# Optimization experiments

Measured on AMD Instinct MI355X. Metric: run time of the kernel, lower is better.

## Reference

```python
import jax, jax.numpy as jnp
import numpy as np

N_CELLS_PER_SIDE = 16
MAX_K = 32
N_HEADS = 8
CHUNK = 128

_NEIGHBOR_OFFSETS = jnp.array([[-1, -1], [-1, 0], [-1, 1], [0, -1], [0, 0], [0, 1], [1, -1], [1, 0], [1, 1]], dtype=jnp.int32)


def cell_lookup(query_pos, cell_map, pos_min, pos_range):
    B, S, _ = query_pos.shape
    mpc = cell_map.shape[1]
    normalized = (query_pos - pos_min) / pos_range
    cell_xy = jnp.clip((normalized * N_CELLS_PER_SIDE).astype(jnp.int32), 0, N_CELLS_PER_SIDE - 1)
    nb = jnp.clip(cell_xy[:, :, None, :] + _NEIGHBOR_OFFSETS[None, None, :, :], 0, N_CELLS_PER_SIDE - 1)
    nidx = nb[..., 0] * N_CELLS_PER_SIDE + nb[..., 1]
    cand = cell_map[nidx].reshape(B, S, 9 * mpc)
    valid = cand >= 0
    return jnp.where(valid, cand, 0), valid


def threshold_gate(scores, tau, max_k):
    raw = scores - tau
    gate = jnp.where(raw > 0, raw, 1e-8 * jnp.exp(raw))
    eg = jnp.exp(gate) - 1.0
    k = min(max_k, scores.shape[-1])
    tv, _ = jax.lax.top_k(eg, k)
    eg = jnp.where(eg >= tv[:, :, -1:], eg, 0.0)
    gs = eg.sum(axis=-1, keepdims=True) + 1e-8
    strength = jnp.tanh(eg.max(axis=-1, keepdims=True))
    return eg / gs * strength


def setup_inputs() -> dict:
    key = jax.random.key(0)
    ks = jax.random.split(key, 16)
    B, S, D, N, P = 2, 1024, 512, 4096, 2
    n_cells, mpc = N_CELLS_PER_SIDE ** 2, 32
    return {
        "x": jax.random.normal(ks[0], (B, S, D), jnp.float32),
        "qk_pos": jax.random.uniform(ks[1], (B, S, P), jnp.float32),
        "v_pos": jax.random.uniform(ks[2], (B, S, P), jnp.float32),
        "tau_Q": jax.random.uniform(ks[3], (B, S, 1), jnp.float32),
        "tau_K": jax.random.uniform(ks[4], (B, S, 1), jnp.float32),
        "tau_V": jax.random.uniform(ks[5], (B, S, 1), jnp.float32),
        "qk_neurons": jax.random.normal(ks[6], (N, D), jnp.float32) / np.float32(np.sqrt(D)),
        "v_neurons": jax.random.normal(ks[7], (N, D), jnp.float32) / np.float32(np.sqrt(D)),
        "npos_qk": jax.random.uniform(ks[8], (N, P), jnp.float32),
        "npos_v": jax.random.uniform(ks[9], (N, P), jnp.float32),
        "cell_map_qk": jax.random.randint(ks[10], (n_cells, mpc), 0, N, jnp.int32),
        "cell_map_v": jax.random.randint(ks[11], (n_cells, mpc), 0, N, jnp.int32),
        "pos_min": jnp.zeros((P,), jnp.float32),
        "pos_range": jnp.ones((P,), jnp.float32),
        "expand_O": jax.random.normal(ks[12], (D, D), jnp.float32) * 0.02,
    }


def reference(x, qk_pos, v_pos, tau_Q, tau_K, tau_V, qk_neurons, v_neurons, npos_qk, npos_v, cell_map_qk, cell_map_v, pos_min, pos_range, expand_O):
    B, S, D = x.shape
    # full-sequence spatial cell lookup (small int tensors)
    ci_qk, m_qk = cell_lookup(qk_pos, cell_map_qk, pos_min, pos_range)
    ci_v, m_v = cell_lookup(v_pos, cell_map_v, pos_min, pos_range)
    ci_qk = jax.lax.stop_gradient(ci_qk)
    ci_v = jax.lax.stop_gradient(ci_v)
    nc = S // CHUNK  # S chosen divisible by CHUNK (no padding path needed)

    def chunks(a):
        return a.reshape(B, nc, CHUNK, *a.shape[2:]).swapaxes(0, 1)

    inp = tuple(map(chunks, (x, qk_pos, v_pos, tau_Q, tau_K, tau_V, ci_qk, m_qk, ci_v, m_v)))

    def step(carry, c):
        x_c, qkp, vp, tq, tk, tv, i_qk, mk, i_v, mv = c
        cand_qk = qk_neurons[i_qk]  # [B,C,n_cand,D]
        cand_v = v_neurons[i_v]
        act_qk = jnp.einsum('bsd,bsnd->bsn', x_c, cand_qk)
        act_v = jnp.einsum('bsd,bsnd->bsn', x_c, cand_v)
        s_qk = jnp.where(mk, act_qk, -1e9)
        s_v = jnp.where(mv, act_v, -1e9)
        gQ = threshold_gate(s_qk, tq, MAX_K)
        gK = threshold_gate(s_qk, tk, MAX_K)
        gV = threshold_gate(s_v, tv, MAX_K)
        Q_c = jnp.einsum('bsn,bsnd->bsd', act_qk * gQ * mk, cand_qk)
        K_c = jnp.einsum('bsn,bsnd->bsd', act_qk * gK * mk, cand_qk)
        V_c = jnp.einsum('bsn,bsnd->bsd', act_v * gV * mv, cand_v)
        pd_qk = jnp.sum((qkp[:, :, None, :] - npos_qk[i_qk]) ** 2, axis=-1)
        pl_qk = (jax.lax.stop_gradient(gQ) * pd_qk * mk).sum() / (mk.sum() + 1e-8)
        pd_v = jnp.sum((vp[:, :, None, :] - npos_v[i_v]) ** 2, axis=-1)
        pl_v = (jax.lax.stop_gradient(gV) * pd_v * mv).sum() / (mv.sum() + 1e-8)
        return carry, (Q_c, K_c, V_c, pl_qk + pl_v)

    _, (Qs, Ks, Vs, pls) = jax.lax.scan(step, 0, inp)

    def merge(a):
        return a.swapaxes(0, 1).reshape(B, S, D)

    Q, K, V = merge(Qs), merge(Ks), merge(Vs)
    pos_loss = pls.mean()  # == sum / n_chunks

    dh = D // N_HEADS
    Qh = Q.reshape(B, S, N_HEADS, dh).transpose(0, 2, 1, 3)
    Kh = K.reshape(B, S, N_HEADS, dh).transpose(0, 2, 1, 3)
    Vh = V.reshape(B, S, N_HEADS, dh).transpose(0, 2, 1, 3)
    scores = jnp.einsum('bhsd,bhtd->bhst', Qh, Kh) / jnp.sqrt(jnp.float32(dh))
    causal = jnp.tril(jnp.ones((S, S), dtype=jnp.bool_))
    scores = jnp.where(causal, scores, jnp.finfo(scores.dtype).min)
    attn = jax.nn.softmax(scores, axis=-1)
    out = jnp.einsum('bhst,bhtd->bhsd', attn, Vh)
    out = out.transpose(0, 2, 1, 3).reshape(B, S, D)
    out = out @ expand_O
    return out, pos_loss
```

## Files before the change

### kernel.cpp

```cpp
#include <hip/hip_runtime.h>
#include <math.h>

#define B_ 2
#define S_ 1024
#define D_ 512
#define N_ 4096
#define H_ 8
#define DH_ 64
#define NCAND 288
#define TOPK 32
#define NTOK (B_*S_)
#define NG2 1152

#define NROWS 16384
#define NSLOT_BH 8704
#define NSLOTS (16*NSLOT_BH)

typedef __attribute__((ext_vector_type(8))) short short8;
typedef __attribute__((ext_vector_type(4))) float f32x4;

__device__ __forceinline__ float wave_sum(float v) {
    #pragma unroll
    for (int o = 32; o; o >>= 1) v += __shfl_xor(v, o);
    return v;
}
__device__ __forceinline__ float wave_max(float v) {
    #pragma unroll
    for (int o = 32; o; o >>= 1) v = fmaxf(v, __shfl_xor(v, o));
    return v;
}
__device__ __forceinline__ ushort f2b_rn(float f) {
    unsigned u = __float_as_uint(f);
    return (ushort)((u + 0x7FFFu + ((u >> 16) & 1u)) >> 16);
}
__device__ __forceinline__ float b2f(ushort h) {
    return __uint_as_float(((unsigned)h) << 16);
}
__device__ __forceinline__ int swzi(int row, int c8) {
    return row * 64 + ((c8 ^ (row & 7)) << 3);
}

__global__ __launch_bounds__(1024) void sort_tokens_kernel(
    const float* __restrict__ qk_pos, const float* __restrict__ v_pos,
    const float* __restrict__ pos_min, const float* __restrict__ pos_range,
    int* __restrict__ order_qk, int* __restrict__ order_v,
    int2* __restrict__ desc_qk, int2* __restrict__ desc_v,
    float* __restrict__ posacc)
{
    __shared__ int hist[256], tmp[256], offs[256], startc[256], gcnt[256];
    const int t = threadIdx.x;
    const int pass = blockIdx.x;
    if (pass == 0 && t < 32) posacc[t] = 0.f;
    const float pm0 = pos_min[0], pm1 = pos_min[1];
    const float pr0 = pos_range[0], pr1 = pos_range[1];
    const float* pos = pass ? v_pos : qk_pos;
    int* order = pass ? order_v : order_qk;
    int2* desc = pass ? desc_v : desc_qk;
    if (t < NG2) desc[t] = make_int2(0, 0);
    if (t + 1024 < NG2) desc[t + 1024] = make_int2(0, 0);
    if (t < 256) hist[t] = 0;
    __syncthreads();
    int cell[2];
    #pragma unroll
    for (int k = 0; k < 2; k++) {
        int tok = t + k * 1024;
        float p0 = pos[tok * 2], p1 = pos[tok * 2 + 1];
        int cx = min(max((int)((p0 - pm0) / pr0 * 16.f), 0), 15);
        int cy = min(max((int)((p1 - pm1) / pr1 * 16.f), 0), 15);
        cell[k] = cx * 16 + cy;
        atomicAdd(&hist[cell[k]], 1);
    }
    __syncthreads();
    if (t < 256) tmp[t] = hist[t];
    __syncthreads();
    for (int d = 1; d < 256; d <<= 1) {
        int v = 0;
        if (t < 256 && t >= d) v = tmp[t - d];
        __syncthreads();
        if (t < 256) tmp[t] += v;
        __syncthreads();
    }
    if (t < 256) {
        startc[t] = tmp[t] - hist[t];
        offs[t]   = startc[t];
        gcnt[t]   = (hist[t] + 1) >> 1;
    }
    __syncthreads();
    #pragma unroll
    for (int k = 0; k < 2; k++) {
        int tok = t + k * 1024;
        int p = atomicAdd(&offs[cell[k]], 1);
        order[p] = tok;
    }
    __syncthreads();
    if (t < 256) tmp[t] = gcnt[t];
    __syncthreads();
    for (int d = 1; d < 256; d <<= 1) {
        int v = 0;
        if (t < 256 && t >= d) v = tmp[t - d];
        __syncthreads();
        if (t < 256) tmp[t] += v;
        __syncthreads();
    }
    if (t < 256) {
        int g0 = tmp[t] - gcnt[t];
        for (int k = 0; k < gcnt[t]; k++)
            desc[g0 + k] = make_int2(startc[t] + 2 * k, min(2, hist[t] - 2 * k));
    }
}

__global__ __launch_bounds__(256) void qkv_fused(
    const int2* __restrict__ desc_qk, const int* __restrict__ order_qk,
    const int2* __restrict__ desc_v,  const int* __restrict__ order_v,
    const float* __restrict__ x,
    const float* __restrict__ qk_pos, const float* __restrict__ v_pos,
    const float* __restrict__ tauQ, const float* __restrict__ tauK,
    const float* __restrict__ tauV,
    const float* __restrict__ qk_neurons, const float* __restrict__ v_neurons,
    const float* __restrict__ npos_qk, const float* __restrict__ npos_v,
    const int* __restrict__ cm_qk, const int* __restrict__ cm_v,
    const float* __restrict__ pos_min, const float* __restrict__ pos_range,
    float* __restrict__ Q, float* __restrict__ K, float* __restrict__ V,
    float* __restrict__ posacc)
{
    const int bid = blockIdx.x;
    const int role = bid & 1;
    const int g = bid >> 1;
    const int gid = (g & 7) * 144 + (g >> 3);
    const int2 dsc = role ? desc_v[gid] : desc_qk[gid];
    const int gstart = dsc.x, count = dsc.y;
    if (count == 0) return;

    const int*   order   = role ? order_v   : order_qk;
    const float* pose    = role ? v_pos     : qk_pos;
    const float* neurons = role ? v_neurons : qk_neurons;
    const float* npos    = role ? npos_v    : npos_qk;
    const int*   cmap    = role ? cm_v      : cm_qk;

    __shared__ int   idx[NCAND];
    __shared__ float msk[NCAND];
    __shared__ float act[2][NCAND];
    __shared__ int   ci[2][NCAND];
    __shared__ float cw1[2][NCAND], cw2[2][NCAND];
    __shared__ int   toks[2], cnt2[2];
    __shared__ float red[2][2][4];
    __shared__ float redc;

    const int t = threadIdx.x, wid = t >> 6, lane = t & 63;
    const int sub = lane & 15, grp = lane >> 4;
    if (t < 2) { toks[t] = order[gstart + min(t, count - 1)]; cnt2[t] = 0; }
    __syncthreads();
    const int token0 = toks[0];

    const float pm0 = pos_min[0], pm1 = pos_min[1];
    const float pr0 = pos_range[0], pr1 = pos_range[1];
    {
        const float p0 = pose[token0 * 2], p1 = pose[token0 * 2 + 1];
        const int cx = min(max((int)((p0 - pm0) / pr0 * 16.f), 0), 15);
        const int cy = min(max((int)((p1 - pm1) / pr1 * 16.f), 0), 15);
        for (int c = t; c < NCAND; c += 256) {
            int o = c >> 5, ms = c & 31;
            int nx = min(max(cx + o / 3 - 1, 0), 15), ny = min(max(cy + o % 3 - 1, 0), 15);
            int cand = cmap[(nx * 16 + ny) * 32 + ms];
            idx[c] = cand >= 0 ? cand : 0;
            msk[c] = cand >= 0 ? 1.f : 0.f;
        }
    }
    __syncthreads();

    float4 xr0[8], xr1[8];
    {
        const float4* xp0 = (const float4*)(x + (size_t)toks[0] * D_);
        const float4* xp1 = (const float4*)(x + (size_t)toks[1] * D_);
        #pragma unroll
        for (int k = 0; k < 8; k++) {
            xr0[k] = xp0[k * 16 + sub];
            xr1[k] = xp1[k * 16 + sub];
        }
    }

    const int cb = wid * 72;
    for (int u = 0; u < 72; u += 4) {
        const int c = cb + u + grp;
        const float4* rp = (const float4*)(neurons + (size_t)idx[c] * D_);
        float a0 = 0.f, a1 = 0.f, b0 = 0.f, b1 = 0.f;
        #pragma unroll
        for (int k = 0; k < 8; k += 2) {
            float4 r0 = rp[k * 16 + sub];
            float4 r1 = rp[(k + 1) * 16 + sub];
            a0 += xr0[k].x*r0.x + xr0[k].y*r0.y + xr0[k].z*r0.z + xr0[k].w*r0.w;
            a1 += xr1[k].x*r0.x + xr1[k].y*r0.y + xr1[k].z*r0.z + xr1[k].w*r0.w;
            b0 += xr0[k+1].x*r1.x + xr0[k+1].y*r1.y + xr0[k+1].z*r1.z + xr0[k+1].w*r1.w;
            b1 += xr1[k+1].x*r1.x + xr1[k+1].y*r1.y + xr1[k+1].z*r1.z + xr1[k+1].w*r1.w;
        }
        float f0 = a0 + b0, f1 = a1 + b1;
        #pragma unroll
        for (int o = 1; o <= 8; o <<= 1) {
            f0 += __shfl_xor(f0, o);
            f1 += __shfl_xor(f1, o);
        }
        if (sub == 0) {
            const float mv = msk[c];
            act[0][c] = (mv != 0.f) ? f0 : -1e9f;
            act[1][c] = (mv != 0.f) ? f1 : -1e9f;
        }
    }
    __syncthreads();

    const int tk = wid >> 1, sw = wid & 1, tt = t & 127;
    const int token = toks[tk];

    if (sw == 0) {
        unsigned ej[5];
        #pragma unroll
        for (int k = 0; k < 5; k++) {
            int j = lane + 64 * k;
            float f = (j < NCAND) ? act[tk][j] : -1e30f;
            unsigned uu = __float_as_uint(f);
            ej[k] = (uu & 0x80000000u) ? ~uu : (uu | 0x80000000u);
        }
        unsigned T = 0u;
        for (int bit = 31; bit >= 0; bit--) {
            const unsigned cand = T | (1u << bit);
            int c = 0;
            #pragma unroll
            for (int k = 0; k < 5; k++)
                c += __popcll(__ballot(ej[k] >= cand));
            if (c >= TOPK) T = cand;
        }
        int base = 0;
        const unsigned long long below = (lane == 0) ? 0ull
                                       : (~0ull >> (64 - lane));
        #pragma unroll
        for (int k = 0; k < 5; k++) {
            const unsigned long long mk2 = __ballot(ej[k] >= T);
            if (ej[k] >= T) {
                int pos = base + __popcll(mk2 & below);
                ci[tk][pos] = lane + 64 * k;
            }
            base += __popcll(mk2);
        }
        if (lane == 0) cnt2[tk] = base;
    }
    if (wid == 0) {
        float cmv = 0.f;
        for (int c = lane; c < NCAND; c += 64) cmv += msk[c];
        cmv = wave_sum(cmv);
        if (lane == 0) redc = cmv;
    }
    __syncthreads();
    const float cm = redc;
    const int n = cnt2[tk];

    if (role == 0) {
        const float tq = tauQ[token], tkk = tauK[token];
        float sQ = 0.f, sK = 0.f, mQ = 0.f, mK = 0.f;
        for (int p = tt; p < n; p += 128) {
            float s = act[tk][ci[tk][p]];
            float rq = s - tq;
            float gq = (rq > 0.f) ? rq : 1e-8f * __expf(rq);
            float egq = __expf(gq) - 1.f;
            float rk = s - tkk;
            float gk = (rk > 0.f) ? rk : 1e-8f * __expf(rk);
            float egk = __expf(gk) - 1.f;
            cw1[tk][p] = egq; cw2[tk][p] = egk;
            sQ += egq; sK += egk;
            mQ = fmaxf(mQ, egq); mK = fmaxf(mK, egk);
        }
        sQ = wave_sum(sQ); mQ = wave_max(mQ);
        sK = wave_sum(sK); mK = wave_max(mK);
        if (lane == 0) {
            red[tk][sw][0] = sQ; red[tk][sw][1] = mQ;
            red[tk][sw][2] = sK; red[tk][sw][3] = mK;
        }
        __syncthreads();
        const float scQ = tanhf(fmaxf(red[tk][0][1], red[tk][1][1]))
                        / (red[tk][0][0] + red[tk][1][0] + 1e-8f);
        const float scK = tanhf(fmaxf(red[tk][0][3], red[tk][1][3]))
                        / (red[tk][0][2] + red[tk][1][2] + 1e-8f);
        __syncthreads();

        const float qp0 = pose[token * 2], qp1 = pose[token * 2 + 1];
        float plq = 0.f;
        for (int p = tt; p < n; p += 128) {
            int e = ci[tk][p];
            int id = idx[e];
            float m = msk[e], a = act[tk][e];
            float gq = cw1[tk][p] * scQ;
            cw1[tk][p] = a * gq * m;
            cw2[tk][p] = a * cw2[tk][p] * scK * m;
            ci[tk][p] = id;
            float d0 = qp0 - npos[id * 2], d1 = qp1 - npos[id * 2 + 1];
            plq += gq * (d0 * d0 + d1 * d1) * m;
        }
        plq = wave_sum(plq);
        if (lane == 0) red[tk][sw][0] = plq;
        __syncthreads();
        if (tt == 0 && tk < count) {
            int chunk = (token & 1023) >> 7;
            atomicAdd(&posacc[chunk], red[tk][0][0] + red[tk][1][0]);
            atomicAdd(&posacc[8 + chunk], cm);
        }

        if (tk < count) {
            float4 qa = {0,0,0,0}, ka = {0,0,0,0};
            int p = 0;
            for (; p + 1 < n; p += 2) {
                const float4 rA = *(const float4*)(neurons + (size_t)ci[tk][p] * D_ + tt * 4);
                const float4 rB = *(const float4*)(neurons + (size_t)ci[tk][p + 1] * D_ + tt * 4);
                const float wA = cw1[tk][p], bA = cw2[tk][p];
                const float wB = cw1[tk][p + 1], bB = cw2[tk][p + 1];
                qa.x += wA * rA.x + wB * rB.x; qa.y += wA * rA.y + wB * rB.y;
                qa.z += wA * rA.z + wB * rB.z; qa.w += wA * rA.w + wB * rB.w;
                ka.x += bA * rA.x + bB * rB.x; ka.y += bA * rA.y + bB * rB.y;
                ka.z += bA * rA.z + bB * rB.z; ka.w += bA * rA.w + bB * rB.w;
            }
            if (p < n) {
                const float4 rA = *(const float4*)(neurons + (size_t)ci[tk][p] * D_ + tt * 4);
                const float wA = cw1[tk][p], bA = cw2[tk][p];
                qa.x += wA * rA.x; qa.y += wA * rA.y; qa.z += wA * rA.z; qa.w += wA * rA.w;
                ka.x += bA * rA.x; ka.y += bA * rA.y; ka.z += bA * rA.z; ka.w += bA * rA.w;
            }
            *(float4*)(Q + (size_t)token * D_ + tt * 4) = qa;
            *(float4*)(K + (size_t)token * D_ + tt * 4) = ka;
        }
    } else {
        const float tv = tauV[token];
        float sV = 0.f, mV = 0.f;
        for (int p = tt; p < n; p += 128) {
            float s = act[tk][ci[tk][p]];
            float rv = s - tv;
            float gv = (rv > 0.f) ? rv : 1e-8f * __expf(rv);
            float egv = __expf(gv) - 1.f;
            cw1[tk][p] = egv;
            sV += egv; mV = fmaxf(mV, egv);
        }
        sV = wave_sum(sV); mV = wave_max(mV);
        if (lane == 0) { red[tk][sw][0] = sV; red[tk][sw][1] = mV; }
        __syncthreads();
        const float scV = tanhf(fmaxf(red[tk][0][1], red[tk][1][1]))
                        / (red[tk][0][0] + red[tk][1][0] + 1e-8f);
        __syncthreads();

        const float vp0 = pose[token * 2], vp1 = pose[token * 2 + 1];
        float plv = 0.f;
        for (int p = tt; p < n; p += 128) {
            int e = ci[tk][p];
            int id = idx[e];
            float m = msk[e], a = act[tk][e];
            float gv = cw1[tk][p] * scV;
            cw1[tk][p] = a * gv * m;
            ci[tk][p] = id;
            float d0 = vp0 - npos[id * 2], d1 = vp1 - npos[id * 2 + 1];
            plv += gv * (d0 * d0 + d1 * d1) * m;
        }
        plv = wave_sum(plv);
        if (lane == 0) red[tk][sw][0] = plv;
        __syncthreads();
        if (tt == 0 && tk < count) {
            int chunk = (token & 1023) >> 7;
            atomicAdd(&posacc[16 + chunk], red[tk][0][0] + red[tk][1][0]);
            atomicAdd(&posacc[24 + chunk], cm);
        }

        if (tk < count) {
            float4 va = {0,0,0,0};
            int p = 0;
            for (; p + 1 < n; p += 2) {
                const float4 rA = *(const float4*)(neurons + (size_t)ci[tk][p] * D_ + tt * 4);
                const float4 rB = *(const float4*)(neurons + (size_t)ci[tk][p + 1] * D_ + tt * 4);
                const float wA = cw1[tk][p], wB = cw1[tk][p + 1];
                va.x += wA * rA.x + wB * rB.x; va.y += wA * rA.y + wB * rB.y;
                va.z += wA * rA.z + wB * rB.z; va.w += wA * rA.w + wB * rB.w;
            }
            if (p < n) {
                const float4 rA = *(const float4*)(neurons + (size_t)ci[tk][p] * D_ + tt * 4);
                const float wA = cw1[tk][p];
                va.x += wA * rA.x; va.y += wA * rA.y; va.z += wA * rA.z; va.w += wA * rA.w;
            }
            *(float4*)(V + (size_t)token * D_ + tt * 4) = va;
        }
    }
}

__global__ __launch_bounds__(256) void wprep_kernel(
    const float* __restrict__ W, ushort* __restrict__ Wth, ushort* __restrict__ Wtl)
{
    __shared__ float tile[64][65];
    const int bx = blockIdx.x & 7, by = blockIdx.x >> 3;
    const int t = threadIdx.x;
    const int r = t >> 4, c4 = (t & 15) * 4;
    #pragma unroll
    for (int rr = 0; rr < 64; rr += 16) {
        const float4 v = *(const float4*)(W + (size_t)(by * 64 + rr + r) * 512 + bx * 64 + c4);
        *(float4*)&tile[rr + r][c4] = v;
    }
    __syncthreads();
    #pragma unroll
    for (int cc = 0; cc < 64; cc += 16) {
        const int c = cc + r;
        ushort h[4], l[4];
        #pragma unroll
        for (int i = 0; i < 4; i++) {
            float f = tile[c4 + i][c];
            h[i] = f2b_rn(f);
            l[i] = f2b_rn(f - b2f(h[i]));
        }
        *(uint2*)&Wth[(size_t)(bx * 64 + c) * 512 + by * 64 + c4] = *(uint2*)h;
        *(uint2*)&Wtl[(size_t)(bx * 64 + c) * 512 + by * 64 + c4] = *(uint2*)l;
    }
}

__global__ __launch_bounds__(256, 2) void attn_partial_kernel(
    const float* __restrict__ Q, const float* __restrict__ K,
    const float* __restrict__ V,
    float* __restrict__ pm, float* __restrict__ pl, float* __restrict__ po)
{
    const int xx = blockIdx.x & 7;
    int kq = blockIdx.x >> 3;
    const int bh = xx + 8 * (kq >= 72);
    kq = (kq >= 72) ? kq - 72 : kq;
    int rblk = 0;
    while (kq >= 2 * (rblk + 1)) { kq -= 2 * (rblk + 1); rblk++; }
    const int sp = kq;
    const int b = bh >> 3, h = bh & 7;
    const int j0 = sp * 64;
    const int rbase = rblk * 128;

    __shared__ __align__(16) ushort sKhi[64 * 64], sKlo[64 * 64];
    __shared__ __align__(16) ushort sVthi[64 * 64], sVtlo[64 * 64];
    __shared__ __align__(16) float sPool[8192];

    const int t = threadIdx.x;
    const int w = t >> 6, lane = t & 63;
    const int g = lane >> 4, ln = lane & 15;

    {
        const int srow = t >> 2, scol = (t & 3) << 4;
        const float* Kg = K + ((size_t)(b * S_ + j0 + srow)) * D_ + h * DH_ + scol;
        const float* Vg = V + ((size_t)(b * S_ + j0 + srow)) * D_ + h * DH_ + scol;
        union { float4 f4[4]; float f[16]; } kf, vf;
        kf.f4[0] = *(const float4*)(Kg);
        kf.f4[1] = *(const float4*)(Kg + 4);
        kf.f4[2] = *(const float4*)(Kg + 8);
        kf.f4[3] = *(const float4*)(Kg + 12);
        vf.f4[0] = *(const float4*)(Vg);
        vf.f4[1] = *(const float4*)(Vg + 4);
        vf.f4[2] = *(const float4*)(Vg + 8);
        vf.f4[3] = *(const float4*)(Vg + 12);
        union { uint4 d[2]; ushort u[16]; } uh, ul;
        #pragma unroll
        for (int i = 0; i < 16; i++) {
            uh.u[i] = f2b_rn(kf.f[i]);
            ul.u[i] = f2b_rn(kf.f[i] - b2f(uh.u[i]));
        }
        const int c8 = (t & 3) << 1;
        *(uint4*)&sKhi[swzi(srow, c8)]     = uh.d[0];
        *(uint4*)&sKhi[swzi(srow, c8 + 1)] = uh.d[1];
        *(uint4*)&sKlo[swzi(srow, c8)]     = ul.d[0];
        *(uint4*)&sKlo[swzi(srow, c8 + 1)] = ul.d[1];
        #pragma unroll
        for (int i = 0; i < 16; i++) sPool[srow * 65 + scol + i] = vf.f[i];
    }
    __syncthreads();
    {
        const int drow = t >> 2, kcol = (t & 3) << 4;
        union { uint4 d[2]; ushort u[16]; } uh, ul;
        #pragma unroll
        for (int i = 0; i < 16; i++) {
            const float f = sPool[(kcol + i) * 65 + drow];
            uh.u[i] = f2b_rn(f);
            ul.u[i] = f2b_rn(f - b2f(uh.u[i]));
        }
        const int c8 = (t & 3) << 1;
        *(uint4*)&sVthi[swzi(drow, c8)]     = uh.d[0];
        *(uint4*)&sVthi[swzi(drow, c8 + 1)] = uh.d[1];
        *(uint4*)&sVtlo[swzi(drow, c8)]     = ul.d[0];
        *(uint4*)&sVtlo[swzi(drow, c8 + 1)] = ul.d[1];
    }
    __syncthreads();

    const int wrow = rbase + w * 32;
    if (wrow + 31 < j0) return;

    ushort* sPw = (ushort*)sPool + w * 4096;

    short8 qhi[2][2], qlo[2][2];
    #pragma unroll
    for (int qt = 0; qt < 2; qt++) {
        const int qrow = wrow + qt * 16 + ln;
        const float* Qg = Q + ((size_t)(b * S_ + qrow)) * D_ + h * DH_ + g * 8;
        #pragma unroll
        for (int ds = 0; ds < 2; ds++) {
            union { float4 f4[2]; float f[8]; } qf;
            qf.f4[0] = *(const float4*)(Qg + ds * 32);
            qf.f4[1] = *(const float4*)(Qg + ds * 32 + 4);
            union { short8 v; ushort u[8]; } uh, ul;
            #pragma unroll
            for (int i = 0; i < 8; i++) {
                uh.u[i] = f2b_rn(qf.f[i]);
                ul.u[i] = f2b_rn(qf.f[i] - b2f(uh.u[i]));
            }
            qhi[qt][ds] = uh.v; qlo[qt][ds] = ul.v;
        }
    }

    const f32x4 fzero = {0.f, 0.f, 0.f, 0.f};
    f32x4 sT[2][4];
    #pragma unroll
    for (int qt = 0; qt < 2; qt++)
        #pragma unroll
        for (int kt = 0; kt < 4; kt++)
            sT[qt][kt] = fzero;
    #pragma unroll
    for (int ds = 0; ds < 2; ds++) {
        #pragma unroll
        for (int kt = 0; kt < 4; kt++) {
            const int krow = kt * 16 + ln;
            const short8 khi = *(const short8*)&sKhi[swzi(krow, ds * 4 + g)];
            const short8 klo = *(const short8*)&sKlo[swzi(krow, ds * 4 + g)];
            #pragma unroll
            for (int qt = 0; qt < 2; qt++) {
                sT[qt][kt] = __builtin_amdgcn_mfma_f32_16x16x32_bf16(khi, qhi[qt][ds], sT[qt][kt], 0, 0, 0);
                sT[qt][kt] = __builtin_amdgcn_mfma_f32_16x16x32_bf16(khi, qlo[qt][ds], sT[qt][kt], 0, 0, 0);
                sT[qt][kt] = __builtin_amdgcn_mfma_f32_16x16x32_bf16(klo, qhi[qt][ds], sT[qt][kt], 0, 0, 0);
            }
        }
    }

    #pragma unroll
    for (int qt = 0; qt < 2; qt++) {
        const int qg = wrow + qt * 16 + ln;
        float pv[16];
        float mq = -1e30f;
        #pragma unroll
        for (int kt = 0; kt < 4; kt++)
            #pragma unroll
            for (int r = 0; r < 4; r++) {
                const int kg = j0 + kt * 16 + g * 4 + r;
                float s = sT[qt][kt][r] * 0.125f;
                s = (kg <= qg) ? s : -1e30f;
                pv[kt * 4 + r] = s;
                mq = fmaxf(mq, s);
            }
        mq = fmaxf(mq, __shfl_xor(mq, 16));
        mq = fmaxf(mq, __shfl_xor(mq, 32));
        const float base = (mq < -1e29f) ? 0.f : mq;
        float lq = 0.f;
        #pragma unroll
        for (int i = 0; i < 16; i++) {
            const float e = __expf(pv[i] - base);
            pv[i] = e;
            lq += e;
        }
        lq += __shfl_xor(lq, 16);
        lq += __shfl_xor(lq, 32);

        const int qrow = qt * 16 + ln;
        #pragma unroll
        for (int kt = 0; kt < 4; kt++) {
            union { uint2 d; ushort u[4]; } h4, l4;
            #pragma unroll
            for (int r = 0; r < 4; r++) {
                const float f = pv[kt * 4 + r];
                h4.u[r] = f2b_rn(f);
                l4.u[r] = f2b_rn(f - b2f(h4.u[r]));
            }
            const int c8 = kt * 2 + (g >> 1);
            const int idx = qrow * 64 + ((c8 ^ (qrow & 7)) << 3) + ((g & 1) << 2);
            *(uint2*)&sPw[idx] = h4.d;
            *(uint2*)&sPw[2048 + idx] = l4.d;
        }
        if (g == 0 && qg >= j0) {
            const int gr = qg >> 6;
            const size_t slot = (size_t)bh * NSLOT_BH + 32 * gr * (gr + 1)
                              + (size_t)(qg & 63) * (gr + 1) + sp;
            pm[slot] = mq; pl[slot] = lq;
        }
    }

    f32x4 ot[4][2];
    #pragma unroll
    for (int dt = 0; dt < 4; dt++)
        #pragma unroll
        for (int qt = 0; qt < 2; qt++)
            ot[dt][qt] = fzero;
    #pragma unroll
    for (int ks = 0; ks < 2; ks++) {
        short8 pfh[2], pfl[2];
        #pragma unroll
        for (int qt = 0; qt < 2; qt++) {
            const int qrow = qt * 16 + ln;
            const int idx = qrow * 64 + (((ks * 4 + g) ^ (qrow & 7)) << 3);
            pfh[qt] = *(const short8*)&sPw[idx];
            pfl[qt] = *(const short8*)&sPw[2048 + idx];
        }
        #pragma unroll
        for (int dt = 0; dt < 4; dt++) {
            const int drow = dt * 16 + ln;
            const short8 vh = *(const short8*)&sVthi[swzi(drow, ks * 4 + g)];
            const short8 vl = *(const short8*)&sVtlo[swzi(drow, ks * 4 + g)];
            #pragma unroll
            for (int qt = 0; qt < 2; qt++) {
                ot[dt][qt] = __builtin_amdgcn_mfma_f32_16x16x32_bf16(vh, pfh[qt], ot[dt][qt], 0, 0, 0);
                ot[dt][qt] = __builtin_amdgcn_mfma_f32_16x16x32_bf16(vh, pfl[qt], ot[dt][qt], 0, 0, 0);
                ot[dt][qt] = __builtin_amdgcn_mfma_f32_16x16x32_bf16(vl, pfh[qt], ot[dt][qt], 0, 0, 0);
            }
        }
    }

    #pragma unroll
    for (int qt = 0; qt < 2; qt++) {
        const int qg = wrow + qt * 16 + ln;
        if (qg < j0) continue;
        const int gr = qg >> 6;
        const size_t slot = (size_t)bh * NSLOT_BH + 32 * gr * (gr + 1)
                          + (size_t)(qg & 63) * (gr + 1) + sp;
        float* od = po + slot * 64 + g * 4;
        #pragma unroll
        for (int dt = 0; dt < 4; dt++)
            *(f32x4*)(od + dt * 16) = ot[dt][qt];
    }
}

__global__ __launch_bounds__(256) void attn_combine_kernel(
    const float* __restrict__ pm, const float* __restrict__ pl,
    const float* __restrict__ po, float* __restrict__ AO)
{
    const int gth = blockIdx.x * 256 + threadIdx.x;
    const int r = gth >> 6, d = gth & 63;
    const int i = r & 1023, bh = r >> 10;
    const int b = bh >> 3, h = bh & 7;
    const int g = i >> 6;
    const int ns = g + 1;
    const size_t slot0 = (size_t)bh * NSLOT_BH + 32 * g * (g + 1)
                       + (size_t)(i & 63) * (g + 1);
    float mstar = -INFINITY, lstar = 0.f, ostar = 0.f;
    for (int s = 0; s < ns; s++) {
        const float mi = pm[slot0 + s];
        const float nm = fmaxf(mstar, mi);
        const float a = __expf(mstar - nm);
        const float w = __expf(mi - nm);
        lstar = lstar * a + pl[slot0 + s] * w;
        ostar = ostar * a + po[(slot0 + s) * 64 + d] * w;
        mstar = nm;
    }
    AO[((size_t)(b * S_ + i)) * D_ + h * DH_ + d] = ostar / lstar;
}

__global__ __launch_bounds__(256) void proj_kernel(
    const float* __restrict__ A,
    const ushort* __restrict__ Wth, const ushort* __restrict__ Wtl,
    float* __restrict__ out)
{
    const int tb = (blockIdx.x >> 4) * 64;
    const int cb = (blockIdx.x & 15) * 32;
    const int t = threadIdx.x, w = t >> 6, lane = t & 63;
    const int ln = lane & 15, ko = (lane >> 4) * 8;
    const int tok = tb + w * 16 + ln;

    const f32x4 fz = {0.f, 0.f, 0.f, 0.f};
    f32x4 acc[2];
    acc[0] = fz; acc[1] = fz;

    const float* Ap = A + (size_t)tok * 512 + ko;
    #pragma unroll 4
    for (int ks = 0; ks < 512; ks += 32) {
        union { float4 f4[2]; float f[8]; } af;
        af.f4[0] = *(const float4*)(Ap + ks);
        af.f4[1] = *(const float4*)(Ap + ks + 4);
        union { short8 v; ushort u[8]; } ah, al;
        #pragma unroll
        for (int i = 0; i < 8; i++) {
            ah.u[i] = f2b_rn(af.f[i]);
            al.u[i] = f2b_rn(af.f[i] - b2f(ah.u[i]));
        }
        #pragma unroll
        for (int ct = 0; ct < 2; ct++) {
            const size_t wb = (size_t)(cb + ct * 16 + ln) * 512 + ks + ko;
            const short8 bh = *(const short8*)(Wth + wb);
            const short8 bl = *(const short8*)(Wtl + wb);
            acc[ct] = __builtin_amdgcn_mfma_f32_16x16x32_bf16(ah.v, bh, acc[ct], 0, 0, 0);
            acc[ct] = __builtin_amdgcn_mfma_f32_16x16x32_bf16(al.v, bh, acc[ct], 0, 0, 0);
            acc[ct] = __builtin_amdgcn_mfma_f32_16x16x32_bf16(ah.v, bl, acc[ct], 0, 0, 0);
        }
    }
    #pragma unroll
    for (int ct = 0; ct < 2; ct++) {
        #pragma unroll
        for (int r = 0; r < 4; r++) {
            const int row = tb + w * 16 + (lane >> 4) * 4 + r;
            out[(size_t)row * 512 + cb + ct * 16 + ln] = acc[ct][r];
        }
    }
}

__global__ void ploss_kernel(const float* __restrict__ acc, float* __restrict__ out) {
    float ssum = 0.f;
    for (int c = 0; c < 8; c++) {
        ssum += acc[c]      / (acc[8 + c]  + 1e-8f);
        ssum += acc[16 + c] / (acc[24 + c] + 1e-8f);
    }
    out[0] = ssum * 0.125f;
}

extern "C" void kernel_launch(void* const* d_in, const int* in_sizes, int n_in,
                              void* d_out, int out_size, void* d_ws, size_t ws_size,
                              hipStream_t stream) {
    const float* x          = (const float*)d_in[0];
    const float* qk_pos     = (const float*)d_in[1];
    const float* v_pos      = (const float*)d_in[2];
    const float* tauQ       = (const float*)d_in[3];
    const float* tauK       = (const float*)d_in[4];
    const float* tauV       = (const float*)d_in[5];
    const float* qk_neurons = (const float*)d_in[6];
    const float* v_neurons  = (const float*)d_in[7];
    const float* npos_qk    = (const float*)d_in[8];
    const float* npos_v     = (const float*)d_in[9];
    const int*   cm_qk      = (const int*)d_in[10];
    const int*   cm_v       = (const int*)d_in[11];
    const float* pos_min    = (const float*)d_in[12];
    const float* pos_range  = (const float*)d_in[13];
    const float* expand_O   = (const float*)d_in[14];

    float* ws = (float*)d_ws;
    const size_t TDf = (size_t)NTOK * D_;
    float* Q   = ws;
    float* K   = ws + TDf;
    float* V   = ws + 2 * TDf;
    float* AO  = ws + 3 * TDf;
    float* acc = ws + 4 * TDf;
    int*   order_qk = (int*)(ws + 4 * TDf + 64);
    int*   order_v  = order_qk + NTOK;
    int2*  desc_qk  = (int2*)(order_v + NTOK);
    int2*  desc_v   = desc_qk + NG2;
    const size_t head = 4 * TDf + 64 + 2 * NTOK + 4 * NG2;

    float* pm = ws + head;
    float* pl = pm + (size_t)NSLOTS;
    float* po = pl + (size_t)NSLOTS;
    ushort* Wth = (ushort*)(po + (size_t)NSLOTS * 64);
    ushort* Wtl = Wth + 512 * 512;

    float* out = (float*)d_out;

    sort_tokens_kernel<<<2, 1024, 0, stream>>>(qk_pos, v_pos, pos_min, pos_range,
                                               order_qk, order_v, desc_qk, desc_v,
                                               acc);
    wprep_kernel<<<64, 256, 0, stream>>>(expand_O, Wth, Wtl);
    qkv_fused<<<2 * NG2, 256, 0, stream>>>(desc_qk, order_qk, desc_v, order_v,
                                           x, qk_pos, v_pos, tauQ, tauK, tauV,
                                           qk_neurons, v_neurons, npos_qk, npos_v,
                                           cm_qk, cm_v, pos_min, pos_range,
                                           Q, K, V, acc);
    attn_partial_kernel<<<1152, 256, 0, stream>>>(Q, K, V, pm, pl, po);
    attn_combine_kernel<<<(NROWS * 64) / 256, 256, 0, stream>>>(pm, pl, po, AO);
    proj_kernel<<<512, 256, 0, stream>>>(AO, Wth, Wtl, out);
    ploss_kernel<<<1, 1, 0, stream>>>(acc, out + TDf);
}
```

Before: 256.0 us.

## Process two key tiles per attention block with online softmax; fuse small kernels

Each attention partial block now walks two 64-key halves of a 128-key split, keeping a running max and sum (online softmax). This halves the number of split slots that must be written and later merged, and the grid shrinks from 1152 to 576 blocks. The weight-prep work is folded into the sort kernel as extra blocks, and the pos-loss reduction is folded into the projection kernel, removing two launches. The cost is fewer blocks to fill the GPU and more serial work per block in attention.

```diff
diff --git a/kernel.cpp b/kernel.cpp
--- a/kernel.cpp
+++ b/kernel.cpp
@@ -13,7 +13,7 @@
 #define NG2 1152
 
 #define NROWS 16384
-#define NSLOT_BH 8704
+#define NSLOT_BH 4608
 #define NSLOTS (16*NSLOT_BH)
 
 typedef __attribute__((ext_vector_type(8))) short short8;
@@ -40,16 +40,51 @@
     return row * 64 + ((c8 ^ (row & 7)) << 3);
 }
 
-__global__ __launch_bounds__(1024) void sort_tokens_kernel(
+__global__ __launch_bounds__(1024) void sort_wprep_kernel(
     const float* __restrict__ qk_pos, const float* __restrict__ v_pos,
     const float* __restrict__ pos_min, const float* __restrict__ pos_range,
     int* __restrict__ order_qk, int* __restrict__ order_v,
     int2* __restrict__ desc_qk, int2* __restrict__ desc_v,
-    float* __restrict__ posacc)
+    float* __restrict__ posacc,
+    const float* __restrict__ W, ushort* __restrict__ Wth, ushort* __restrict__ Wtl)
 {
     __shared__ int hist[256], tmp[256], offs[256], startc[256], gcnt[256];
+    __shared__ float tile[64][65];
     const int t = threadIdx.x;
-    const int pass = blockIdx.x;
+    const int bid = blockIdx.x;
+
+    if (bid >= 2) {
+        const int bb = bid - 2;
+        const int bx = bb & 7, by = bb >> 3;
+        if (t < 256) {
+            const int r = t >> 4, c4 = (t & 15) * 4;
+            #pragma unroll
+            for (int rr = 0; rr < 64; rr += 16) {
+                const float4 v = *(const float4*)(W + (size_t)(by * 64 + rr + r) * 512 + bx * 64 + c4);
+                *(float4*)&tile[rr + r][c4] = v;
+            }
+        }
+        __syncthreads();
+        if (t < 256) {
+            const int r = t >> 4, c4 = (t & 15) * 4;
+            #pragma unroll
+            for (int cc = 0; cc < 64; cc += 16) {
+                const int c = cc + r;
+                ushort h[4], l[4];
+                #pragma unroll
+                for (int i = 0; i < 4; i++) {
+                    float f = tile[c4 + i][c];
+                    h[i] = f2b_rn(f);
+                    l[i] = f2b_rn(f - b2f(h[i]));
+                }
+                *(uint2*)&Wth[(size_t)(bx * 64 + c) * 512 + by * 64 + c4] = *(uint2*)h;
+                *(uint2*)&Wtl[(size_t)(bx * 64 + c) * 512 + by * 64 + c4] = *(uint2*)l;
+            }
+        }
+        return;
+    }
+
+    const int pass = bid;
     if (pass == 0 && t < 32) posacc[t] = 0.f;
     const float pm0 = pos_min[0], pm1 = pos_min[1];
     const float pr0 = pos_range[0], pr1 = pos_range[1];
@@ -383,48 +418,18 @@
     }
 }
 
-__global__ __launch_bounds__(256) void wprep_kernel(
-    const float* __restrict__ W, ushort* __restrict__ Wth, ushort* __restrict__ Wtl)
-{
-    __shared__ float tile[64][65];
-    const int bx = blockIdx.x & 7, by = blockIdx.x >> 3;
-    const int t = threadIdx.x;
-    const int r = t >> 4, c4 = (t & 15) * 4;
-    #pragma unroll
-    for (int rr = 0; rr < 64; rr += 16) {
-        const float4 v = *(const float4*)(W + (size_t)(by * 64 + rr + r) * 512 + bx * 64 + c4);
-        *(float4*)&tile[rr + r][c4] = v;
-    }
-    __syncthreads();
-    #pragma unroll
-    for (int cc = 0; cc < 64; cc += 16) {
-        const int c = cc + r;
-        ushort h[4], l[4];
-        #pragma unroll
-        for (int i = 0; i < 4; i++) {
-            float f = tile[c4 + i][c];
-            h[i] = f2b_rn(f);
-            l[i] = f2b_rn(f - b2f(h[i]));
-        }
-        *(uint2*)&Wth[(size_t)(bx * 64 + c) * 512 + by * 64 + c4] = *(uint2*)h;
-        *(uint2*)&Wtl[(size_t)(bx * 64 + c) * 512 + by * 64 + c4] = *(uint2*)l;
-    }
-}
-
 __global__ __launch_bounds__(256, 2) void attn_partial_kernel(
     const float* __restrict__ Q, const float* __restrict__ K,
     const float* __restrict__ V,
     float* __restrict__ pm, float* __restrict__ pl, float* __restrict__ po)
 {
-    const int xx = blockIdx.x & 7;
-    int kq = blockIdx.x >> 3;
-    const int bh = xx + 8 * (kq >= 72);
-    kq = (kq >= 72) ? kq - 72 : kq;
+    const int bh = blockIdx.x & 15;
+    int kq = blockIdx.x >> 4;
     int rblk = 0;
-    while (kq >= 2 * (rblk + 1)) { kq -= 2 * (rblk + 1); rblk++; }
+    while (kq >= rblk + 1) { kq -= rblk + 1; rblk++; }
     const int sp = kq;
     const int b = bh >> 3, h = bh & 7;
-    const int j0 = sp * 64;
+    const int j0 = sp * 128;
     const int rbase = rblk * 128;
 
     __shared__ __align__(16) ushort sKhi[64 * 64], sKlo[64 * 64];
@@ -434,56 +439,7 @@
     const int t = threadIdx.x;
     const int w = t >> 6, lane = t & 63;
     const int g = lane >> 4, ln = lane & 15;
-
-    {
-        const int srow = t >> 2, scol = (t & 3) << 4;
-        const float* Kg = K + ((size_t)(b * S_ + j0 + srow)) * D_ + h * DH_ + scol;
-        const float* Vg = V + ((size_t)(b * S_ + j0 + srow)) * D_ + h * DH_ + scol;
-        union { float4 f4[4]; float f[16]; } kf, vf;
-        kf.f4[0] = *(const float4*)(Kg);
-        kf.f4[1] = *(const float4*)(Kg + 4);
-        kf.f4[2] = *(const float4*)(Kg + 8);
-        kf.f4[3] = *(const float4*)(Kg + 12);
-        vf.f4[0] = *(const float4*)(Vg);
-        vf.f4[1] = *(const float4*)(Vg + 4);
-        vf.f4[2] = *(const float4*)(Vg + 8);
-        vf.f4[3] = *(const float4*)(Vg + 12);
-        union { uint4 d[2]; ushort u[16]; } uh, ul;
-        #pragma unroll
-        for (int i = 0; i < 16; i++) {
-            uh.u[i] = f2b_rn(kf.f[i]);
-            ul.u[i] = f2b_rn(kf.f[i] - b2f(uh.u[i]));
-        }
-        const int c8 = (t & 3) << 1;
-        *(uint4*)&sKhi[swzi(srow, c8)]     = uh.d[0];
-        *(uint4*)&sKhi[swzi(srow, c8 + 1)] = uh.d[1];
-        *(uint4*)&sKlo[swzi(srow, c8)]     = ul.d[0];
-        *(uint4*)&sKlo[swzi(srow, c8 + 1)] = ul.d[1];
-        #pragma unroll
-        for (int i = 0; i < 16; i++) sPool[srow * 65 + scol + i] = vf.f[i];
-    }
-    __syncthreads();
-    {
-        const int drow = t >> 2, kcol = (t & 3) << 4;
-        union { uint4 d[2]; ushort u[16]; } uh, ul;
-        #pragma unroll
-        for (int i = 0; i < 16; i++) {
-            const float f = sPool[(kcol + i) * 65 + drow];
-            uh.u[i] = f2b_rn(f);
-            ul.u[i] = f2b_rn(f - b2f(uh.u[i]));
-        }
-        const int c8 = (t & 3) << 1;
-        *(uint4*)&sVthi[swzi(drow, c8)]     = uh.d[0];
-        *(uint4*)&sVthi[swzi(drow, c8 + 1)] = uh.d[1];
-        *(uint4*)&sVtlo[swzi(drow, c8)]     = ul.d[0];
-        *(uint4*)&sVtlo[swzi(drow, c8 + 1)] = ul.d[1];
-    }
-    __syncthreads();
-
     const int wrow = rbase + w * 32;
-    if (wrow + 31 < j0) return;
-
-    ushort* sPw = (ushort*)sPool + w * 4096;
 
     short8 qhi[2][2], qlo[2][2];
     #pragma unroll
@@ -506,24 +462,163 @@
     }
 
     const f32x4 fzero = {0.f, 0.f, 0.f, 0.f};
-    f32x4 sT[2][4];
+    f32x4 ot[4][2];
     #pragma unroll
-    for (int qt = 0; qt < 2; qt++)
-        #pragma unroll
-        for (int kt = 0; kt < 4; kt++)
-            sT[qt][kt] = fzero;
-    #pragma unroll
-    for (int ds = 0; ds < 2; ds++) {
-        #pragma unroll
-        for (int kt = 0; kt < 4; kt++) {
-            const int krow = kt * 16 + ln;
-            const short8 khi = *(const short8*)&sKhi[swzi(krow, ds * 4 + g)];
-            const short8 klo = *(const short8*)&sKlo[swzi(krow, ds * 4 + g)];
+    for (int dt = 0; dt < 4; dt++)
+        #pragma unroll
+        for (int qt = 0; qt < 2; qt++)
+            ot[dt][qt] = fzero;
+    float m_run[2] = {-1e30f, -1e30f};
+    float l_run[2] = {0.f, 0.f};
+
+    for (int half = 0; half < 2; half++) {
+        const int j0h = j0 + half * 64;
+        __syncthreads();
+
+        {
+            const int srow = t >> 2, scol = (t & 3) << 4;
+            const float* Kg = K + ((size_t)(b * S_ + j0h + srow)) * D_ + h * DH_ + scol;
+            const float* Vg = V + ((size_t)(b * S_ + j0h + srow)) * D_ + h * DH_ + scol;
+            union { float4 f4[4]; float f[16]; } kf, vf;
+            kf.f4[0] = *(const float4*)(Kg);
+            kf.f4[1] = *(const float4*)(Kg + 4);
+            kf.f4[2] = *(const float4*)(Kg + 8);
+            kf.f4[3] = *(const float4*)(Kg + 12);
+            vf.f4[0] = *(const float4*)(Vg);
+            vf.f4[1] = *(const float4*)(Vg + 4);
+            vf.f4[2] = *(const float4*)(Vg + 8);
+            vf.f4[3] = *(const float4*)(Vg + 12);
+            union { uint4 d[2]; ushort u[16]; } uh, ul;
+            #pragma unroll
+            for (int i = 0; i < 16; i++) {
+                uh.u[i] = f2b_rn(kf.f[i]);
+                ul.u[i] = f2b_rn(kf.f[i] - b2f(uh.u[i]));
+            }
+            const int c8 = (t & 3) << 1;
+            *(uint4*)&sKhi[swzi(srow, c8)]     = uh.d[0];
+            *(uint4*)&sKhi[swzi(srow, c8 + 1)] = uh.d[1];
+            *(uint4*)&sKlo[swzi(srow, c8)]     = ul.d[0];
+            *(uint4*)&sKlo[swzi(srow, c8 + 1)] = ul.d[1];
+            #pragma unroll
+            for (int i = 0; i < 16; i++) sPool[srow * 65 + scol + i] = vf.f[i];
+        }
+        __syncthreads();
+        {
+            const int drow = t >> 2, kcol = (t & 3) << 4;
+            union { uint4 d[2]; ushort u[16]; } uh, ul;
+            #pragma unroll
+            for (int i = 0; i < 16; i++) {
+                const float f = sPool[(kcol + i) * 65 + drow];
+                uh.u[i] = f2b_rn(f);
+                ul.u[i] = f2b_rn(f - b2f(uh.u[i]));
+            }
+            const int c8 = (t & 3) << 1;
+            *(uint4*)&sVthi[swzi(drow, c8)]     = uh.d[0];
+            *(uint4*)&sVthi[swzi(drow, c8 + 1)] = uh.d[1];
+            *(uint4*)&sVtlo[swzi(drow, c8)]     = ul.d[0];
+            *(uint4*)&sVtlo[swzi(drow, c8 + 1)] = ul.d[1];
+        }
+        __syncthreads();
+
+        if (wrow + 31 < j0h) continue;
+
+        ushort* sPw = (ushort*)sPool + w * 4096;
+
+        f32x4 sT[2][4];
+        #pragma unroll
+        for (int qt = 0; qt < 2; qt++)
+            #pragma unroll
+            for (int kt = 0; kt < 4; kt++)
+                sT[qt][kt] = fzero;
+        #pragma unroll
+        for (int ds = 0; ds < 2; ds++) {
+            #pragma unroll
+            for (int kt = 0; kt < 4; kt++) {
+                const int krow = kt * 16 + ln;
+                const short8 khi = *(const short8*)&sKhi[swzi(krow, ds * 4 + g)];
+                const short8 klo = *(const short8*)&sKlo[swzi(krow, ds * 4 + g)];
+                #pragma unroll
+                for (int qt = 0; qt < 2; qt++) {
+                    sT[qt][kt] = __builtin_amdgcn_mfma_f32_16x16x32_bf16(khi, qhi[qt][ds], sT[qt][kt], 0, 0, 0);
+                    sT[qt][kt] = __builtin_amdgcn_mfma_f32_16x16x32_bf16(khi, qlo[qt][ds], sT[qt][kt], 0, 0, 0);
+                    sT[qt][kt] = __builtin_amdgcn_mfma_f32_16x16x32_bf16(klo, qhi[qt][ds], sT[qt][kt], 0, 0, 0);
+                }
+            }
+        }
+
+        #pragma unroll
+        for (int qt = 0; qt < 2; qt++) {
+            const int qg = wrow + qt * 16 + ln;
+            float pv[16];
+            float mq = -1e30f;
+            #pragma unroll
+            for (int kt = 0; kt < 4; kt++)
+                #pragma unroll
+                for (int r = 0; r < 4; r++) {
+                    const int kg = j0h + kt * 16 + g * 4 + r;
+                    float s = sT[qt][kt][r] * 0.125f;
+                    s = (kg <= qg) ? s : -1e30f;
+                    pv[kt * 4 + r] = s;
+                    mq = fmaxf(mq, s);
+                }
+            mq = fmaxf(mq, __shfl_xor(mq, 16));
+            mq = fmaxf(mq, __shfl_xor(mq, 32));
+            const float mN = fmaxf(m_run[qt], mq);
+            const float base = (mN < -1e29f) ? 0.f : mN;
+            const float a = __expf(m_run[qt] - mN);
+            m_run[qt] = mN;
+            float lq = 0.f;
+            #pragma unroll
+            for (int i = 0; i < 16; i++) {
+                const float e = __expf(pv[i] - base);
+                pv[i] = e;
+                lq += e;
+            }
+            lq += __shfl_xor(lq, 16);
+            lq += __shfl_xor(lq, 32);
+            l_run[qt] = l_run[qt] * a + lq;
+            #pragma unroll
+            for (int dt = 0; dt < 4; dt++)
+                ot[dt][qt] *= a;
+
+            const int qrow = qt * 16 + ln;
+            #pragma unroll
+            for (int kt = 0; kt < 4; kt++) {
+                union { uint2 d; ushort u[4]; } h4, l4;
+                #pragma unroll
+                for (int r = 0; r < 4; r++) {
+                    const float f = pv[kt * 4 + r];
+                    h4.u[r] = f2b_rn(f);
+                    l4.u[r] = f2b_rn(f - b2f(h4.u[r]));
+                }
+                const int c8 = kt * 2 + (g >> 1);
+                const int idx = qrow * 64 + ((c8 ^ (qrow & 7)) << 3) + ((g & 1) << 2);
+                *(uint2*)&sPw[idx] = h4.d;
+                *(uint2*)&sPw[2048 + idx] = l4.d;
+            }
+        }
+
+        #pragma unroll
+        for (int ks = 0; ks < 2; ks++) {
+            short8 pfh[2], pfl[2];
             #pragma unroll
             for (int qt = 0; qt < 2; qt++) {
-                sT[qt][kt] = __builtin_amdgcn_mfma_f32_16x16x32_bf16(khi, qhi[qt][ds], sT[qt][kt], 0, 0, 0);
-                sT[qt][kt] = __builtin_amdgcn_mfma_f32_16x16x32_bf16(khi, qlo[qt][ds], sT[qt][kt], 0, 0, 0);
-                sT[qt][kt] = __builtin_amdgcn_mfma_f32_16x16x32_bf16(klo, qhi[qt][ds], sT[qt][kt], 0, 0, 0);
+                const int qrow = qt * 16 + ln;
+                const int idx = qrow * 64 + (((ks * 4 + g) ^ (qrow & 7)) << 3);
+                pfh[qt] = *(const short8*)&sPw[idx];
+                pfl[qt] = *(const short8*)&sPw[2048 + idx];
+            }
+            #pragma unroll
+            for (int dt = 0; dt < 4; dt++) {
+                const int drow = dt * 16 + ln;
+                const short8 vh = *(const short8*)&sVthi[swzi(drow, ks * 4 + g)];
+                const short8 vl = *(const short8*)&sVtlo[swzi(drow, ks * 4 + g)];
+                #pragma unroll
+                for (int qt = 0; qt < 2; qt++) {
+                    ot[dt][qt] = __builtin_amdgcn_mfma_f32_16x16x32_bf16(vh, pfh[qt], ot[dt][qt], 0, 0, 0);
+                    ot[dt][qt] = __builtin_amdgcn_mfma_f32_16x16x32_bf16(vh, pfl[qt], ot[dt][qt], 0, 0, 0);
+                    ot[dt][qt] = __builtin_amdgcn_mfma_f32_16x16x32_bf16(vl, pfh[qt], ot[dt][qt], 0, 0, 0);
+                }
             }
         }
     }
@@ -531,91 +626,10 @@
     #pragma unroll
     for (int qt = 0; qt < 2; qt++) {
         const int qg = wrow + qt * 16 + ln;
-        float pv[16];
-        float mq = -1e30f;
-        #pragma unroll
-        for (int kt = 0; kt < 4; kt++)
-            #pragma unroll
-            for (int r = 0; r < 4; r++) {
-                const int kg = j0 + kt * 16 + g * 4 + r;
-                float s = sT[qt][kt][r] * 0.125f;
-                s = (kg <= qg) ? s : -1e30f;
-                pv[kt * 4 + r] = s;
-                mq = fmaxf(mq, s);
-            }
-        mq = fmaxf(mq, __shfl_xor(mq, 16));
-        mq = fmaxf(mq, __shfl_xor(mq, 32));
-        const float base = (mq < -1e29f) ? 0.f : mq;
-        float lq = 0.f;
-        #pragma unroll
-        for (int i = 0; i < 16; i++) {
-            const float e = __expf(pv[i] - base);
-            pv[i] = e;
-            lq += e;
-        }
-        lq += __shfl_xor(lq, 16);
-        lq += __shfl_xor(lq, 32);
-
-        const int qrow = qt * 16 + ln;
-        #pragma unroll
-        for (int kt = 0; kt < 4; kt++) {
-            union { uint2 d; ushort u[4]; } h4, l4;
-            #pragma unroll
-            for (int r = 0; r < 4; r++) {
-                const float f = pv[kt * 4 + r];
-                h4.u[r] = f2b_rn(f);
-                l4.u[r] = f2b_rn(f - b2f(h4.u[r]));
-            }
-            const int c8 = kt * 2 + (g >> 1);
-            const int idx = qrow * 64 + ((c8 ^ (qrow & 7)) << 3) + ((g & 1) << 2);
-            *(uint2*)&sPw[idx] = h4.d;
-            *(uint2*)&sPw[2048 + idx] = l4.d;
-        }
-        if (g == 0 && qg >= j0) {
-            const int gr = qg >> 6;
-            const size_t slot = (size_t)bh * NSLOT_BH + 32 * gr * (gr + 1)
-                              + (size_t)(qg & 63) * (gr + 1) + sp;
-            pm[slot] = mq; pl[slot] = lq;
-        }
-    }
-
-    f32x4 ot[4][2];
-    #pragma unroll
-    for (int dt = 0; dt < 4; dt++)
-        #pragma unroll
-        for (int qt = 0; qt < 2; qt++)
-            ot[dt][qt] = fzero;
-    #pragma unroll
-    for (int ks = 0; ks < 2; ks++) {
-        short8 pfh[2], pfl[2];
-        #pragma unroll
-        for (int qt = 0; qt < 2; qt++) {
-            const int qrow = qt * 16 + ln;
-            const int idx = qrow * 64 + (((ks * 4 + g) ^ (qrow & 7)) << 3);
-            pfh[qt] = *(const short8*)&sPw[idx];
-            pfl[qt] = *(const short8*)&sPw[2048 + idx];
-        }
-        #pragma unroll
-        for (int dt = 0; dt < 4; dt++) {
-            const int drow = dt * 16 + ln;
-            const short8 vh = *(const short8*)&sVthi[swzi(drow, ks * 4 + g)];
-            const short8 vl = *(const short8*)&sVtlo[swzi(drow, ks * 4 + g)];
-            #pragma unroll
-            for (int qt = 0; qt < 2; qt++) {
-                ot[dt][qt] = __builtin_amdgcn_mfma_f32_16x16x32_bf16(vh, pfh[qt], ot[dt][qt], 0, 0, 0);
-                ot[dt][qt] = __builtin_amdgcn_mfma_f32_16x16x32_bf16(vh, pfl[qt], ot[dt][qt], 0, 0, 0);
-                ot[dt][qt] = __builtin_amdgcn_mfma_f32_16x16x32_bf16(vl, pfh[qt], ot[dt][qt], 0, 0, 0);
-            }
-        }
-    }
-
-    #pragma unroll
-    for (int qt = 0; qt < 2; qt++) {
-        const int qg = wrow + qt * 16 + ln;
-        if (qg < j0) continue;
-        const int gr = qg >> 6;
-        const size_t slot = (size_t)bh * NSLOT_BH + 32 * gr * (gr + 1)
-                          + (size_t)(qg & 63) * (gr + 1) + sp;
+        const int g2 = qg >> 7;
+        const size_t slot = (size_t)bh * NSLOT_BH + 64 * g2 * (g2 + 1)
+                          + (size_t)(qg & 127) * (g2 + 1) + sp;
+        if (g == 0) { pm[slot] = m_run[qt]; pl[slot] = l_run[qt]; }
         float* od = po + slot * 64 + g * 4;
         #pragma unroll
         for (int dt = 0; dt < 4; dt++)
@@ -631,10 +645,10 @@
     const int r = gth >> 6, d = gth & 63;
     const int i = r & 1023, bh = r >> 10;
     const int b = bh >> 3, h = bh & 7;
-    const int g = i >> 6;
+    const int g = i >> 7;
     const int ns = g + 1;
-    const size_t slot0 = (size_t)bh * NSLOT_BH + 32 * g * (g + 1)
-                       + (size_t)(i & 63) * (g + 1);
+    const size_t slot0 = (size_t)bh * NSLOT_BH + 64 * g * (g + 1)
+                       + (size_t)(i & 127) * (g + 1);
     float mstar = -INFINITY, lstar = 0.f, ostar = 0.f;
     for (int s = 0; s < ns; s++) {
         const float mi = pm[slot0 + s];
@@ -651,8 +665,17 @@
 __global__ __launch_bounds__(256) void proj_kernel(
     const float* __restrict__ A,
     const ushort* __restrict__ Wth, const ushort* __restrict__ Wtl,
-    float* __restrict__ out)
+    const float* __restrict__ acc,
+    float* __restrict__ out, float* __restrict__ outp)
 {
+    if (blockIdx.x == 0 && threadIdx.x == 0) {
+        float ssum = 0.f;
+        for (int c = 0; c < 8; c++) {
+            ssum += acc[c]      / (acc[8 + c]  + 1e-8f);
+            ssum += acc[16 + c] / (acc[24 + c] + 1e-8f);
+        }
+        outp[0] = ssum * 0.125f;
+    }
     const int tb = (blockIdx.x >> 4) * 64;
     const int cb = (blockIdx.x & 15) * 32;
     const int t = threadIdx.x, w = t >> 6, lane = t & 63;
@@ -660,8 +683,8 @@
     const int tok = tb + w * 16 + ln;
 
     const f32x4 fz = {0.f, 0.f, 0.f, 0.f};
-    f32x4 acc[2];
-    acc[0] = fz; acc[1] = fz;
+    f32x4 acc2[2];
+    acc2[0] = fz; acc2[1] = fz;
 
     const float* Ap = A + (size_t)tok * 512 + ko;
     #pragma unroll 4
@@ -680,9 +703,9 @@
             const size_t wb = (size_t)(cb + ct * 16 + ln) * 512 + ks + ko;
             const short8 bh = *(const short8*)(Wth + wb);
             const short8 bl = *(const short8*)(Wtl + wb);
-            acc[ct] = __builtin_amdgcn_mfma_f32_16x16x32_bf16(ah.v, bh, acc[ct], 0, 0, 0);
-            acc[ct] = __builtin_amdgcn_mfma_f32_16x16x32_bf16(al.v, bh, acc[ct], 0, 0, 0);
-            acc[ct] = __builtin_amdgcn_mfma_f32_16x16x32_bf16(ah.v, bl, acc[ct], 0, 0, 0);
+            acc2[ct] = __builtin_amdgcn_mfma_f32_16x16x32_bf16(ah.v, bh, acc2[ct], 0, 0, 0);
+            acc2[ct] = __builtin_amdgcn_mfma_f32_16x16x32_bf16(al.v, bh, acc2[ct], 0, 0, 0);
+            acc2[ct] = __builtin_amdgcn_mfma_f32_16x16x32_bf16(ah.v, bl, acc2[ct], 0, 0, 0);
         }
     }
     #pragma unroll
@@ -690,18 +713,9 @@
         #pragma unroll
         for (int r = 0; r < 4; r++) {
             const int row = tb + w * 16 + (lane >> 4) * 4 + r;
-            out[(size_t)row * 512 + cb + ct * 16 + ln] = acc[ct][r];
-        }
-    }
-}
-
-__global__ void ploss_kernel(const float* __restrict__ acc, float* __restrict__ out) {
-    float ssum = 0.f;
-    for (int c = 0; c < 8; c++) {
-        ssum += acc[c]      / (acc[8 + c]  + 1e-8f);
-        ssum += acc[16 + c] / (acc[24 + c] + 1e-8f);
-    }
-    out[0] = ssum * 0.125f;
+            out[(size_t)row * 512 + cb + ct * 16 + ln] = acc2[ct][r];
+        }
+    }
 }
 
 extern "C" void kernel_launch(void* const* d_in, const int* in_sizes, int n_in,
@@ -744,17 +758,15 @@
 
     float* out = (float*)d_out;
 
-    sort_tokens_kernel<<<2, 1024, 0, stream>>>(qk_pos, v_pos, pos_min, pos_range,
+    sort_wprep_kernel<<<66, 1024, 0, stream>>>(qk_pos, v_pos, pos_min, pos_range,
                                                order_qk, order_v, desc_qk, desc_v,
-                                               acc);
-    wprep_kernel<<<64, 256, 0, stream>>>(expand_O, Wth, Wtl);
+                                               acc, expand_O, Wth, Wtl);
     qkv_fused<<<2 * NG2, 256, 0, stream>>>(desc_qk, order_qk, desc_v, order_v,
                                            x, qk_pos, v_pos, tauQ, tauK, tauV,
                                            qk_neurons, v_neurons, npos_qk, npos_v,
                                            cm_qk, cm_v, pos_min, pos_range,
                                            Q, K, V, acc);
-    attn_partial_kernel<<<1152, 256, 0, stream>>>(Q, K, V, pm, pl, po);
+    attn_partial_kernel<<<16 * 36, 256, 0, stream>>>(Q, K, V, pm, pl, po);
     attn_combine_kernel<<<(NROWS * 64) / 256, 256, 0, stream>>>(pm, pl, po, AO);
-    proj_kernel<<<512, 256, 0, stream>>>(AO, Wth, Wtl, out);
-    ploss_kernel<<<1, 1, 0, stream>>>(acc, out + TDf);
-}
+    proj_kernel<<<512, 256, 0, stream>>>(AO, Wth, Wtl, acc, out, out + TDf);
+}
```

Result: faster. 247.1 us (median of 2 runs) (-3.5%).
